# Performance work log

Measured on AMD Instinct MI355X. Metric: run time of the kernel, lower is better.

The kernel has to match this reference:

```python
import jax, jax.numpy as jnp
import numpy as np

B, T, V, E, H1, H2 = 256, 512, 50000, 300, 50, 10


def _lstm(xs, mask, W_ih, W_hh, b, hidden):
    """Masked LSTM over time-major xs [T,B,D]. mask [T,B,1]: True = valid step.
    Matches PyTorch gate order (i,f,g,o). Padded steps freeze (h,c), which is
    equivalent to pack_padded_sequence semantics (final hidden = state at last
    valid timestep)."""
    Bn = xs.shape[1]
    h0 = jnp.zeros((Bn, hidden), xs.dtype)
    c0 = jnp.zeros((Bn, hidden), xs.dtype)

    def step(carry, inp):
        h, c = carry
        x_t, m_t = inp
        g = x_t @ W_ih.T + h @ W_hh.T + b  # [B, 4H]
        i, f, gg, o = jnp.split(g, 4, axis=-1)
        c_new = jax.nn.sigmoid(f) * c + jax.nn.sigmoid(i) * jnp.tanh(gg)
        h_new = jax.nn.sigmoid(o) * jnp.tanh(c_new)
        h = jnp.where(m_t, h_new, h)
        c = jnp.where(m_t, c_new, c)
        return (h, c), h

    (hT, _), hs = jax.lax.scan(step, (h0, c0), (xs, mask))
    return hs, hT


def setup_inputs() -> dict:
    key = jax.random.key(0)
    ks = jax.random.split(key, 12)
    x = jax.random.randint(ks[0], (B, T), 0, V, dtype=jnp.int64)
    lengths = jax.random.randint(ks[1], (B,), 1, T + 1, dtype=jnp.int64)
    emb = jax.random.normal(ks[2], (V, E), dtype=jnp.float32)
    s1 = 1.0 / np.sqrt(H1)
    s2 = 1.0 / np.sqrt(H2)
    return {
        "x": x,
        "lengths": lengths,
        "emb": emb,
        "W_ih1": jax.random.uniform(ks[3], (4 * H1, E), jnp.float32, -s1, s1),
        "W_hh1": jax.random.uniform(ks[4], (4 * H1, H1), jnp.float32, -s1, s1),
        "b1": jax.random.uniform(ks[5], (4 * H1,), jnp.float32, -s1, s1),
        "W_ih2": jax.random.uniform(ks[6], (4 * H2, H1), jnp.float32, -s2, s2),
        "W_hh2": jax.random.uniform(ks[7], (4 * H2, H2), jnp.float32, -s2, s2),
        "b2": jax.random.uniform(ks[8], (4 * H2,), jnp.float32, -s2, s2),
        "fc1_w": jax.random.uniform(ks[9], (10, H2), jnp.float32, -s2, s2),
        "fc1_b": jnp.zeros((10,), jnp.float32),
        "fc2_w": jax.random.uniform(ks[10], (1, 10), jnp.float32, -s2, s2),
        "fc2_b": jnp.zeros((1,), jnp.float32),
    }


def reference(x, lengths, emb, W_ih1, W_hh1, b1, W_ih2, W_hh2, b2,
              fc1_w, fc1_b, fc2_w, fc2_b):
    e = emb[x]                                   # [B,T,E]
    xs = jnp.transpose(e, (1, 0, 2))             # time-major [T,B,E]
    mask = (jnp.arange(T)[:, None] < lengths[None, :])[..., None]  # [T,B,1]
    hs1, _ = _lstm(xs, mask, W_ih1, W_hh1, b1, H1)   # [T,B,50]
    _, h2 = _lstm(hs1, mask, W_ih2, W_hh2, b2, H2)   # final hidden [B,10]
    # dropout layers are identity in eval mode
    z = jax.nn.relu(h2 @ fc1_w.T + fc1_b)
    return z @ fc2_w.T + fc2_b                   # [B,1]
```

## Files before the change

kernel.cpp:

```cpp
#include <hip/hip_runtime.h>
#include <hip/hip_bf16.h>

#define BB 256
#define TT 512
#define EE 300
#define G4 200
#define NPAD 208
#define KP 1216
#define KC 64
#define KPD (KP/2)
#define KCD (KC/2)
#define NCH 19
#define NT 13
#define BOFF 8192
#define BUFB 34816

typedef __attribute__((ext_vector_type(8))) short short8v;
typedef __attribute__((ext_vector_type(4))) float float4v;
typedef __attribute__((ext_vector_type(4))) unsigned int uint4v;


__device__ __forceinline__ float sigm(float x) {
    return __builtin_amdgcn_rcpf(1.f + __builtin_amdgcn_exp2f(-1.442695040888963f * x));
}
__device__ __forceinline__ float tanh_(float x) {
    float t = __builtin_amdgcn_exp2f(2.885390081777927f * x);
    return 1.f - 2.f * __builtin_amdgcn_rcpf(t + 1.f);
}
template <int C>
__device__ __forceinline__ float qb(float v) {
    return __int_as_float(__builtin_amdgcn_mov_dpp(__float_as_int(v), C, 0xF, 0xF, true));
}

__device__ __forceinline__ uint2 bfsplit(float a) {
    unsigned u = __float_as_uint(a);
    unsigned rh = (u + 0x7FFFu + ((u >> 16) & 1u)) & 0xFFFF0000u;
    float l = a - __uint_as_float(rh);
    unsigned v = __float_as_uint(l);
    unsigned rl = (v + 0x7FFFu + ((v >> 16) & 1u)) >> 16;
    return make_uint2(rh >> 16, rl);
}

__global__ void wtrans_kernel(const float* __restrict__ W, const float* __restrict__ b1,
                              unsigned* __restrict__ Btg, float* __restrict__ b1p) {
    int e = blockIdx.x;
    int j = threadIdx.x;
    if (j >= NPAD) return;
    float w = 0.f;
    if (j < G4) w = W[((j & 3) * 50 + (j >> 2)) * EE + e];
    uint2 s = bfsplit(w);
    unsigned dw0 = s.x | (s.x << 16);
    unsigned dw1 = s.y | (s.y << 16);
    *(uint2*)(Btg + (size_t)j * KPD + 2 * e) = make_uint2(dw0, dw1);
    if (e == 0) b1p[j] = (j < G4) ? b1[(j & 3) * 50 + (j >> 2)] : 0.f;
}

__global__ __launch_bounds__(256, 2) void proj_kernel(
    const int* __restrict__ x, const int* __restrict__ lengths,
    const float* __restrict__ emb, const unsigned* __restrict__ Btg,
    const float* __restrict__ b1p, float* __restrict__ G1, int b0)
{
    const int b  = b0 + blockIdx.y;
    const int t0 = blockIdx.x * 64;
    const int len = lengths[b];
    if (t0 >= len) return;

    const int tid  = threadIdx.x;
    const int wv   = tid >> 6;
    const int lane = tid & 63;

    __shared__ __align__(16) char lds[2 * BUFB];

    const int arow = tid >> 2;
    const int ag   = tid & 3;
    const float* er = emb + (size_t)x[b * TT + t0 + arow] * EE;

    float4v acc[NT] = {};

    auto stageB = [&](int c, int q) {
        char* base = lds + q * BUFB + BOFF;
        #pragma unroll
        for (int rr = 0; rr < 7; ++rr) {
            if (rr < 6 || tid < 128) {
                int g   = rr * 256 + tid;
                int row = g >> 3, sl = g & 7;
                const unsigned* src = Btg + (size_t)row * KPD + c * KCD
                                      + ((sl ^ (row & 7)) << 2);
                char* dst = base + (rr * 256 + (tid & ~63)) * 16;
                __builtin_amdgcn_global_load_lds(
                    (const __attribute__((address_space(1))) void*)src,
                    (__attribute__((address_space(3))) void*)dst, 16, 0, 0);
            }
        }
    };
    auto loadA = [&](int cc) -> float4 {
        int k0 = cc * 16 + ag * 4;
        if (k0 < EE) return *(const float4*)(er + k0);
        return make_float4(0.f, 0.f, 0.f, 0.f);
    };
    auto writeA = [&](int q, float4 av) {
        uint2 s0 = bfsplit(av.x), s1 = bfsplit(av.y);
        uint2 s2 = bfsplit(av.z), s3 = bfsplit(av.w);
        unsigned p0 = s0.x | (s0.y << 16), p1 = s1.x | (s1.y << 16);
        unsigned p2 = s2.x | (s2.y << 16), p3 = s3.x | (s3.y << 16);
        char* base = lds + q * BUFB + (arow << 7);
        int r7 = arow & 7;
        *(uint4v*)(base + ((( 2 * ag    ) ^ r7) << 4)) = uint4v{p0, p0, p1, p1};
        *(uint4v*)(base + (((2 * ag + 1) ^ r7) << 4)) = uint4v{p2, p2, p3, p3};
    };

    stageB(0, 0);
    float4 aval = loadA(0);
    asm volatile("s_waitcnt vmcnt(0)" ::: "memory");
    writeA(0, aval);
    asm volatile("s_waitcnt lgkmcnt(0)" ::: "memory");
    __builtin_amdgcn_s_barrier();
    __builtin_amdgcn_sched_barrier(0);

    int p = 0;
    for (int c = 0; c < NCH; ++c) {
        const int q = p ^ 1;
        if (c + 1 < NCH) {
            stageB(c + 1, q);
            aval = loadA(c + 1);
        }
        const int r  = lane & 15;
        const int h  = lane >> 4;
        #pragma unroll
        for (int s = 0; s < 2; ++s) {
            const int sw4 = (((4 * s + h) ^ (r & 7)) << 4);
            short8v aF = *(const short8v*)(lds + p * BUFB + ((wv * 16 + r) << 7) + sw4);
            #pragma unroll
            for (int nt = 0; nt < NT; ++nt) {
                short8v bF = *(const short8v*)(lds + p * BUFB + BOFF
                                               + ((nt * 16 + r) << 7) + sw4);
                acc[nt] = __builtin_amdgcn_mfma_f32_16x16x32_bf16(aF, bF, acc[nt], 0, 0, 0);
            }
        }
        if (c + 1 < NCH) {
            asm volatile("s_waitcnt vmcnt(0)" ::: "memory");
            writeA(q, aval);
            asm volatile("s_waitcnt lgkmcnt(0)" ::: "memory");
            __builtin_amdgcn_s_barrier();
            __builtin_amdgcn_sched_barrier(0);
        }
        p = q;
    }

    float* gbase = G1 + ((size_t)blockIdx.y * TT + t0) * G4;
    const int col = lane & 15, rq = lane >> 4;
    #pragma unroll
    for (int nt = 0; nt < NT; ++nt) {
        int jp = nt * 16 + col;
        if (jp < G4) {
            float bias = b1p[jp];
            #pragma unroll
            for (int rr = 0; rr < 4; ++rr)
                gbase[(size_t)(wv * 16 + rq * 4 + rr) * G4 + jp] = acc[nt][rr] + bias;
        }
    }
}

__global__ __launch_bounds__(512, 1) void lstm_kernel(
    const int* __restrict__ lengths,
    const float* __restrict__ W_hh1, const float* __restrict__ W_ih2,
    const float* __restrict__ W_hh2, const float* __restrict__ b2,
    const float* __restrict__ fc1w, const float* __restrict__ fc1b,
    const float* __restrict__ fc2w, const float* __restrict__ fc2b,
    const float* __restrict__ G1, float* __restrict__ out, int b0)
{
    const int bb  = blockIdx.x;
    const int b   = b0 + bb;
    const int tid = threadIdx.x;
    const int len = lengths[b];

    __shared__ __align__(16) float hs[2][72];
    __shared__ __align__(16) float hfin[12];
    __shared__ float zbuf[10];

    if (tid < 72) { hs[0][tid] = 0.f; hs[1][tid] = 0.f; }

    const bool isL1 = (tid < 400);
    const bool isL2 = (tid >= 400 && tid < 480);
    const int  grp  = tid >> 3;
    const int  sub  = tid & 7;
    const int  g    = sub & 3;
    const int  half = sub >> 2;

    float wreg[28];
    float wregb[12];
    #pragma unroll
    for (int k = 0; k < 28; ++k) wreg[k] = 0.f;
    #pragma unroll
    for (int k = 0; k < 12; ++k) wregb[k] = 0.f;
    float base2 = 0.f;

    if (isL1) {
        int row = g * 50 + grp;
        const float* wp = W_hh1 + row * 50 + half * 28;
        int n = half ? 22 : 28;
        for (int k = 0; k < 28; ++k) wreg[k] = (k < n) ? wp[k] : 0.f;
    } else if (isL2) {
        int u = grp - 50;
        int row = g * 10 + u;
        const float* wp = W_ih2 + row * 50 + half * 28;
        int n = half ? 22 : 28;
        for (int k = 0; k < 28; ++k) wreg[k] = (k < n) ? wp[k] : 0.f;
        if (half == 0) {
            const float* wp2 = W_hh2 + row * 10;
            #pragma unroll
            for (int k = 0; k < 10; ++k) wregb[k] = wp2[k];
            base2 = b2[row];
        }
    }

    const bool gld  = isL1 && (half == 0);
    const int  gcol = gld ? (4 * grp + g) : 0;
    const bool wr   = (sub == 0) && (tid < 480);
    const int  slot = isL1 ? grp : (56 + grp - 50);

    float h1v[28], h2v[12];
    #pragma unroll
    for (int k = 0; k < 28; ++k) h1v[k] = 0.f;
    #pragma unroll
    for (int k = 0; k < 12; ++k) h2v[k] = 0.f;

    float c = 0.f;
    const float* g1p = G1 + (size_t)bb * TT * G4;
    float p0 = 0.f, p1 = 0.f, p2 = 0.f;
    if (gld) {
        int t1 = (1 < len) ? 1 : len - 1;
        int t2 = (2 < len) ? 2 : len - 1;
        p0 = g1p[gcol];
        p1 = g1p[(size_t)t1 * G4 + gcol];
        p2 = g1p[(size_t)t2 * G4 + gcol];
    }

    __syncthreads();

    for (int i = 0; i < len; ++i) {
        float base = gld ? p0 : ((isL2 && half == 0) ? base2 : 0.f);
        p0 = p1; p1 = p2;
        if (gld) {
            int tn = (i + 3 < len) ? i + 3 : len - 1;
            p2 = g1p[(size_t)tn * G4 + gcol];
        }

        float s0 = 0.f, s1 = 0.f, s2 = 0.f, s3 = 0.f;
        #pragma unroll
        for (int m = 0; m < 7; ++m) {
            s0 = fmaf(wreg[4*m+0], h1v[4*m+0], s0);
            s1 = fmaf(wreg[4*m+1], h1v[4*m+1], s1);
            s2 = fmaf(wreg[4*m+2], h1v[4*m+2], s2);
            s3 = fmaf(wreg[4*m+3], h1v[4*m+3], s3);
        }
        #pragma unroll
        for (int m = 0; m < 3; ++m) {
            s0 = fmaf(wregb[4*m+0], h2v[4*m+0], s0);
            s1 = fmaf(wregb[4*m+1], h2v[4*m+1], s1);
            s2 = fmaf(wregb[4*m+2], h2v[4*m+2], s2);
            s3 = fmaf(wregb[4*m+3], h2v[4*m+3], s3);
        }
        float t = base + (s0 + s1) + (s2 + s3);
        float full = t + __shfl_xor(t, 4, 64);

        float gi = qb<0x00>(full);
        float gf = qb<0x55>(full);
        float gg = qb<0xAA>(full);
        float go = qb<0xFF>(full);
        float cn = sigm(gf) * c + sigm(gi) * tanh_(gg);
        float hn = sigm(go) * tanh_(cn);
        if (isL2 && i == 0) { cn = 0.f; hn = 0.f; }
        c = cn;
        if (wr) hs[i & 1][slot] = hn;

        asm volatile("s_waitcnt lgkmcnt(0)" ::: "memory");
        __builtin_amdgcn_s_barrier();
        __builtin_amdgcn_sched_barrier(0);

        const float* hb = hs[i & 1] + half * 28;
        #pragma unroll
        for (int m = 0; m < 7; ++m) {
            float4 v = *(const float4*)(hb + 4 * m);
            h1v[4*m+0] = v.x; h1v[4*m+1] = v.y;
            h1v[4*m+2] = v.z; h1v[4*m+3] = v.w;
        }
        if (tid >= 384) {
            const float* hb2 = hs[i & 1] + 56;
            #pragma unroll
            for (int m = 0; m < 3; ++m) {
                float4 v = *(const float4*)(hb2 + 4 * m);
                h2v[4*m+0] = v.x; h2v[4*m+1] = v.y;
                h2v[4*m+2] = v.z; h2v[4*m+3] = v.w;
            }
        }
    }

    {
        float s0 = 0.f, s1 = 0.f, s2 = 0.f, s3 = 0.f;
        #pragma unroll
        for (int m = 0; m < 7; ++m) {
            s0 = fmaf(wreg[4*m+0], h1v[4*m+0], s0);
            s1 = fmaf(wreg[4*m+1], h1v[4*m+1], s1);
            s2 = fmaf(wreg[4*m+2], h1v[4*m+2], s2);
            s3 = fmaf(wreg[4*m+3], h1v[4*m+3], s3);
        }
        #pragma unroll
        for (int m = 0; m < 3; ++m) {
            s0 = fmaf(wregb[4*m+0], h2v[4*m+0], s0);
            s1 = fmaf(wregb[4*m+1], h2v[4*m+1], s1);
            s2 = fmaf(wregb[4*m+2], h2v[4*m+2], s2);
            s3 = fmaf(wregb[4*m+3], h2v[4*m+3], s3);
        }
        float t = ((isL2 && half == 0) ? base2 : 0.f) + (s0 + s1) + (s2 + s3);
        float full = t + __shfl_xor(t, 4, 64);
        float gi = qb<0x00>(full);
        float gf = qb<0x55>(full);
        float gg = qb<0xAA>(full);
        float go = qb<0xFF>(full);
        float cn = sigm(gf) * c + sigm(gi) * tanh_(gg);
        float hn = sigm(go) * tanh_(cn);
        if (isL2 && sub == 0) hfin[grp - 50] = hn;
    }
    __syncthreads();

    if (tid < 10) {
        float s = fc1b[tid];
        #pragma unroll
        for (int e = 0; e < 10; ++e) s = fmaf(fc1w[tid * 10 + e], hfin[e], s);
        zbuf[tid] = s > 0.f ? s : 0.f;
    }
    __syncthreads();
    if (tid == 0) {
        float s = fc2b[0];
        #pragma unroll
        for (int e = 0; e < 10; ++e) s = fmaf(fc2w[e], zbuf[e], s);
        out[b] = s;
    }
}

extern "C" void kernel_launch(void* const* d_in, const int* in_sizes, int n_in,
                              void* d_out, int out_size, void* d_ws, size_t ws_size,
                              hipStream_t stream)
{
    const int*   x     = (const int*)  d_in[0];
    const int*   len   = (const int*)  d_in[1];
    const float* emb   = (const float*)d_in[2];
    const float* W_ih1 = (const float*)d_in[3];
    const float* W_hh1 = (const float*)d_in[4];
    const float* b1    = (const float*)d_in[5];
    const float* W_ih2 = (const float*)d_in[6];
    const float* W_hh2 = (const float*)d_in[7];
    const float* b2    = (const float*)d_in[8];
    const float* fc1w  = (const float*)d_in[9];
    const float* fc1b  = (const float*)d_in[10];
    const float* fc2w  = (const float*)d_in[11];
    const float* fc2b  = (const float*)d_in[12];
    float* out = (float*)d_out;

    const size_t btg_bytes = (size_t)NPAD * KPD * sizeof(unsigned);
    const size_t b1p_off   = btg_bytes;
    const size_t head      = (b1p_off + NPAD * sizeof(float) + 255) & ~255ull;
    const size_t per_b     = (size_t)TT * G4 * sizeof(float);

    unsigned* Btg = (unsigned*)d_ws;
    float*    b1p = (float*)((char*)d_ws + b1p_off);
    float*    G1  = (float*)((char*)d_ws + head);

    size_t avail = ws_size > head ? ws_size - head : 0;
    int chunk = (int)(avail / per_b);
    if (chunk < 1) chunk = 1;
    if (chunk > BB) chunk = BB;

    wtrans_kernel<<<dim3(EE), dim3(256), 0, stream>>>(W_ih1, b1, Btg, b1p);

    for (int b0 = 0; b0 < BB; b0 += chunk) {
        int nb = (BB - b0) < chunk ? (BB - b0) : chunk;
        proj_kernel<<<dim3(TT / 64, nb), dim3(256), 0, stream>>>(
            x, len, emb, Btg, b1p, G1, b0);
        lstm_kernel<<<dim3(nb), dim3(512), 0, stream>>>(
            len, W_hh1, W_ih2, W_hh2, b2, fc1w, fc1b, fc2w, fc2b, G1, out, b0);
    }
}
```

Before: 318.1 us.

## Pack two sequences per LSTM block with two gate rows per thread

Restructures the recurrent LSTM kernel so that each 256-thread block processes two batch elements, one per 128-thread half. Each thread now holds two full weight rows (120 registers) and reads the hidden state directly from shared memory inside the dot product, which removes the split-K shuffle reduction and the per-step register copy of h. Gates are exchanged between thread pairs with a single quad permute. This halves the block count and lowers threads per sequence, at the cost of higher register pressure and steps run to the longer of the two lengths with masking.

```diff
diff --git a/kernel.cpp b/kernel.cpp
--- a/kernel.cpp
+++ b/kernel.cpp
@@ -161,181 +161,163 @@
     }
 }
 
-__global__ __launch_bounds__(512, 1) void lstm_kernel(
+__global__ __launch_bounds__(256, 1) void lstm_kernel(
     const int* __restrict__ lengths,
     const float* __restrict__ W_hh1, const float* __restrict__ W_ih2,
     const float* __restrict__ W_hh2, const float* __restrict__ b2,
     const float* __restrict__ fc1w, const float* __restrict__ fc1b,
     const float* __restrict__ fc2w, const float* __restrict__ fc2b,
-    const float* __restrict__ G1, float* __restrict__ out, int b0)
+    const float* __restrict__ G1, float* __restrict__ out, int b0, int nb)
 {
-    const int bb  = blockIdx.x;
-    const int b   = b0 + bb;
     const int tid = threadIdx.x;
-    const int len = lengths[b];
-
-    __shared__ __align__(16) float hs[2][72];
-    __shared__ __align__(16) float hfin[12];
-    __shared__ float zbuf[10];
-
-    if (tid < 72) { hs[0][tid] = 0.f; hs[1][tid] = 0.f; }
-
-    const bool isL1 = (tid < 400);
-    const bool isL2 = (tid >= 400 && tid < 480);
-    const int  grp  = tid >> 3;
-    const int  sub  = tid & 7;
-    const int  g    = sub & 3;
-    const int  half = sub >> 2;
-
-    float wreg[28];
-    float wregb[12];
+    const int e   = tid >> 7;
+    const int et  = tid & 127;
+    const int u   = et >> 1;
+    const int p   = et & 1;
+    const bool act  = et < 120;
+    const bool isL1 = act && (u < 50);
+    const bool isL2 = act && (u >= 50);
+
+    const int last = b0 + nb - 1;
+    int eg = b0 + blockIdx.x * 2 + e;
+    if (eg > last) eg = last;
+    const int len = lengths[eg];
+    const int ego = b0 + blockIdx.x * 2;
+    const int eg1 = (ego + 1 > last) ? last : ego + 1;
+    const int lenmax = max(lengths[ego], lengths[eg1]);
+
+    __shared__ __align__(16) float hsb[2][2][64];
+    __shared__ float hfin[2][12];
+    __shared__ float zs[2][12];
+    ((float*)hsb)[tid] = 0.f;
+
+    float wA[60], wB[60];
     #pragma unroll
-    for (int k = 0; k < 28; ++k) wreg[k] = 0.f;
-    #pragma unroll
-    for (int k = 0; k < 12; ++k) wregb[k] = 0.f;
-    float base2 = 0.f;
+    for (int k = 0; k < 60; ++k) { wA[k] = 0.f; wB[k] = 0.f; }
+    float baseA0 = 0.f, baseB0 = 0.f;
 
     if (isL1) {
-        int row = g * 50 + grp;
-        const float* wp = W_hh1 + row * 50 + half * 28;
-        int n = half ? 22 : 28;
-        for (int k = 0; k < 28; ++k) wreg[k] = (k < n) ? wp[k] : 0.f;
+        const float* a  = W_hh1 + ((2 * p) * 50 + u) * 50;
+        const float* bp = W_hh1 + ((2 * p + 1) * 50 + u) * 50;
+        #pragma unroll
+        for (int k = 0; k < 50; ++k) { wA[k] = a[k]; wB[k] = bp[k]; }
     } else if (isL2) {
-        int u = grp - 50;
-        int row = g * 10 + u;
-        const float* wp = W_ih2 + row * 50 + half * 28;
-        int n = half ? 22 : 28;
-        for (int k = 0; k < 28; ++k) wreg[k] = (k < n) ? wp[k] : 0.f;
-        if (half == 0) {
-            const float* wp2 = W_hh2 + row * 10;
-            #pragma unroll
-            for (int k = 0; k < 10; ++k) wregb[k] = wp2[k];
-            base2 = b2[row];
-        }
-    }
-
-    const bool gld  = isL1 && (half == 0);
-    const int  gcol = gld ? (4 * grp + g) : 0;
-    const bool wr   = (sub == 0) && (tid < 480);
-    const int  slot = isL1 ? grp : (56 + grp - 50);
-
-    float h1v[28], h2v[12];
-    #pragma unroll
-    for (int k = 0; k < 28; ++k) h1v[k] = 0.f;
-    #pragma unroll
-    for (int k = 0; k < 12; ++k) h2v[k] = 0.f;
-
-    float c = 0.f;
-    const float* g1p = G1 + (size_t)bb * TT * G4;
-    float p0 = 0.f, p1 = 0.f, p2 = 0.f;
-    if (gld) {
+        int u2 = u - 50;
+        int rA = (2 * p) * 10 + u2, rB = (2 * p + 1) * 10 + u2;
+        #pragma unroll
+        for (int k = 0; k < 50; ++k) { wA[k] = W_ih2[rA * 50 + k]; wB[k] = W_ih2[rB * 50 + k]; }
+        #pragma unroll
+        for (int k = 0; k < 10; ++k) { wA[50 + k] = W_hh2[rA * 10 + k]; wB[50 + k] = W_hh2[rB * 10 + k]; }
+        baseA0 = b2[rA]; baseB0 = b2[rB];
+    }
+
+    const int mylen = isL2 ? len + 1 : len;
+    const int gcol  = isL1 ? (4 * u + 2 * p) : 0;
+    const float* g1p = G1 + (size_t)(eg - b0) * TT * G4;
+
+    float2 pf0, pf1, pf2;
+    {
         int t1 = (1 < len) ? 1 : len - 1;
         int t2 = (2 < len) ? 2 : len - 1;
-        p0 = g1p[gcol];
-        p1 = g1p[(size_t)t1 * G4 + gcol];
-        p2 = g1p[(size_t)t2 * G4 + gcol];
-    }
-
+        pf0 = *(const float2*)(g1p + gcol);
+        pf1 = *(const float2*)(g1p + (size_t)t1 * G4 + gcol);
+        pf2 = *(const float2*)(g1p + (size_t)t2 * G4 + gcol);
+    }
+
+    float c = 0.f, hown = 0.f;
     __syncthreads();
 
-    for (int i = 0; i < len; ++i) {
-        float base = gld ? p0 : ((isL2 && half == 0) ? base2 : 0.f);
-        p0 = p1; p1 = p2;
-        if (gld) {
+    int pb = 0;
+    for (int i = 0; i < lenmax; ++i) {
+        float baseA = isL1 ? pf0.x : baseA0;
+        float baseB = isL1 ? pf0.y : baseB0;
+        pf0 = pf1; pf1 = pf2;
+        {
             int tn = (i + 3 < len) ? i + 3 : len - 1;
-            p2 = g1p[(size_t)tn * G4 + gcol];
-        }
-
-        float s0 = 0.f, s1 = 0.f, s2 = 0.f, s3 = 0.f;
-        #pragma unroll
-        for (int m = 0; m < 7; ++m) {
-            s0 = fmaf(wreg[4*m+0], h1v[4*m+0], s0);
-            s1 = fmaf(wreg[4*m+1], h1v[4*m+1], s1);
-            s2 = fmaf(wreg[4*m+2], h1v[4*m+2], s2);
-            s3 = fmaf(wreg[4*m+3], h1v[4*m+3], s3);
-        }
-        #pragma unroll
-        for (int m = 0; m < 3; ++m) {
-            s0 = fmaf(wregb[4*m+0], h2v[4*m+0], s0);
-            s1 = fmaf(wregb[4*m+1], h2v[4*m+1], s1);
-            s2 = fmaf(wregb[4*m+2], h2v[4*m+2], s2);
-            s3 = fmaf(wregb[4*m+3], h2v[4*m+3], s3);
-        }
-        float t = base + (s0 + s1) + (s2 + s3);
-        float full = t + __shfl_xor(t, 4, 64);
-
-        float gi = qb<0x00>(full);
-        float gf = qb<0x55>(full);
-        float gg = qb<0xAA>(full);
-        float go = qb<0xFF>(full);
+            pf2 = *(const float2*)(g1p + (size_t)tn * G4 + gcol);
+        }
+
+        float sA0 = 0.f, sA1 = 0.f, sA2 = 0.f, sA3 = 0.f;
+        float sB0 = 0.f, sB1 = 0.f, sB2 = 0.f, sB3 = 0.f;
+        const float* hb = &hsb[e][pb][0];
+        #pragma unroll
+        for (int m = 0; m < 15; ++m) {
+            float4 hv = *(const float4*)(hb + 4 * m);
+            sA0 = fmaf(wA[4*m+0], hv.x, sA0);
+            sA1 = fmaf(wA[4*m+1], hv.y, sA1);
+            sA2 = fmaf(wA[4*m+2], hv.z, sA2);
+            sA3 = fmaf(wA[4*m+3], hv.w, sA3);
+            sB0 = fmaf(wB[4*m+0], hv.x, sB0);
+            sB1 = fmaf(wB[4*m+1], hv.y, sB1);
+            sB2 = fmaf(wB[4*m+2], hv.z, sB2);
+            sB3 = fmaf(wB[4*m+3], hv.w, sB3);
+        }
+        float tA = baseA + (sA0 + sA1) + (sA2 + sA3);
+        float tB = baseB + (sB0 + sB1) + (sB2 + sB3);
+        float qA = qb<0xB1>(tA);
+        float qB = qb<0xB1>(tB);
+        float gi = p ? qA : tA;
+        float gf = p ? qB : tB;
+        float gg = p ? tA : qA;
+        float go = p ? tB : qB;
         float cn = sigm(gf) * c + sigm(gi) * tanh_(gg);
         float hn = sigm(go) * tanh_(cn);
         if (isL2 && i == 0) { cn = 0.f; hn = 0.f; }
-        c = cn;
-        if (wr) hs[i & 1][slot] = hn;
+        bool upd = (i < mylen);
+        if (upd) c = cn;
+        float hw = upd ? hn : hown;
+        hown = hw;
+        if (act && p == 0) hsb[e][pb ^ 1][u] = hw;
 
         asm volatile("s_waitcnt lgkmcnt(0)" ::: "memory");
         __builtin_amdgcn_s_barrier();
         __builtin_amdgcn_sched_barrier(0);
-
-        const float* hb = hs[i & 1] + half * 28;
-        #pragma unroll
-        for (int m = 0; m < 7; ++m) {
-            float4 v = *(const float4*)(hb + 4 * m);
-            h1v[4*m+0] = v.x; h1v[4*m+1] = v.y;
-            h1v[4*m+2] = v.z; h1v[4*m+3] = v.w;
-        }
-        if (tid >= 384) {
-            const float* hb2 = hs[i & 1] + 56;
-            #pragma unroll
-            for (int m = 0; m < 3; ++m) {
-                float4 v = *(const float4*)(hb2 + 4 * m);
-                h2v[4*m+0] = v.x; h2v[4*m+1] = v.y;
-                h2v[4*m+2] = v.z; h2v[4*m+3] = v.w;
-            }
-        }
+        pb ^= 1;
     }
 
     {
-        float s0 = 0.f, s1 = 0.f, s2 = 0.f, s3 = 0.f;
-        #pragma unroll
-        for (int m = 0; m < 7; ++m) {
-            s0 = fmaf(wreg[4*m+0], h1v[4*m+0], s0);
-            s1 = fmaf(wreg[4*m+1], h1v[4*m+1], s1);
-            s2 = fmaf(wreg[4*m+2], h1v[4*m+2], s2);
-            s3 = fmaf(wreg[4*m+3], h1v[4*m+3], s3);
-        }
-        #pragma unroll
-        for (int m = 0; m < 3; ++m) {
-            s0 = fmaf(wregb[4*m+0], h2v[4*m+0], s0);
-            s1 = fmaf(wregb[4*m+1], h2v[4*m+1], s1);
-            s2 = fmaf(wregb[4*m+2], h2v[4*m+2], s2);
-            s3 = fmaf(wregb[4*m+3], h2v[4*m+3], s3);
-        }
-        float t = ((isL2 && half == 0) ? base2 : 0.f) + (s0 + s1) + (s2 + s3);
-        float full = t + __shfl_xor(t, 4, 64);
-        float gi = qb<0x00>(full);
-        float gf = qb<0x55>(full);
-        float gg = qb<0xAA>(full);
-        float go = qb<0xFF>(full);
+        float sA0 = 0.f, sA1 = 0.f, sA2 = 0.f, sA3 = 0.f;
+        float sB0 = 0.f, sB1 = 0.f, sB2 = 0.f, sB3 = 0.f;
+        const float* hb = &hsb[e][pb][0];
+        #pragma unroll
+        for (int m = 0; m < 15; ++m) {
+            float4 hv = *(const float4*)(hb + 4 * m);
+            sA0 = fmaf(wA[4*m+0], hv.x, sA0);
+            sA1 = fmaf(wA[4*m+1], hv.y, sA1);
+            sA2 = fmaf(wA[4*m+2], hv.z, sA2);
+            sA3 = fmaf(wA[4*m+3], hv.w, sA3);
+            sB0 = fmaf(wB[4*m+0], hv.x, sB0);
+            sB1 = fmaf(wB[4*m+1], hv.y, sB1);
+            sB2 = fmaf(wB[4*m+2], hv.z, sB2);
+            sB3 = fmaf(wB[4*m+3], hv.w, sB3);
+        }
+        float tA = baseA0 + (sA0 + sA1) + (sA2 + sA3);
+        float tB = baseB0 + (sB0 + sB1) + (sB2 + sB3);
+        float qA = qb<0xB1>(tA);
+        float qB = qb<0xB1>(tB);
+        float gi = p ? qA : tA;
+        float gf = p ? qB : tB;
+        float gg = p ? tA : qA;
+        float go = p ? tB : qB;
         float cn = sigm(gf) * c + sigm(gi) * tanh_(gg);
         float hn = sigm(go) * tanh_(cn);
-        if (isL2 && sub == 0) hfin[grp - 50] = hn;
+        float h2f = (len == lenmax) ? hn : hown;
+        if (isL2 && p == 0) hfin[e][u - 50] = h2f;
     }
     __syncthreads();
 
-    if (tid < 10) {
-        float s = fc1b[tid];
-        #pragma unroll
-        for (int e = 0; e < 10; ++e) s = fmaf(fc1w[tid * 10 + e], hfin[e], s);
-        zbuf[tid] = s > 0.f ? s : 0.f;
+    if (et < 10) {
+        float s = fc1b[et];
+        #pragma unroll
+        for (int k = 0; k < 10; ++k) s = fmaf(fc1w[et * 10 + k], hfin[e][k], s);
+        zs[e][et] = s > 0.f ? s : 0.f;
     }
     __syncthreads();
-    if (tid == 0) {
+    if (et == 0) {
         float s = fc2b[0];
         #pragma unroll
-        for (int e = 0; e < 10; ++e) s = fmaf(fc2w[e], zbuf[e], s);
-        out[b] = s;
+        for (int k = 0; k < 10; ++k) s = fmaf(fc2w[k], zs[e][k], s);
+        out[eg] = s;
     }
 }
 
@@ -378,7 +360,7 @@
         int nb = (BB - b0) < chunk ? (BB - b0) : chunk;
         proj_kernel<<<dim3(TT / 64, nb), dim3(256), 0, stream>>>(
             x, len, emb, Btg, b1p, G1, b0);
-        lstm_kernel<<<dim3(nb), dim3(512), 0, stream>>>(
-            len, W_hh1, W_ih2, W_hh2, b2, fc1w, fc1b, fc2w, fc2b, G1, out, b0);
-    }
-}
+        lstm_kernel<<<dim3((nb + 1) / 2), dim3(256), 0, stream>>>(
+            len, W_hh1, W_ih2, W_hh2, b2, fc1w, fc1b, fc2w, fc2b, G1, out, b0, nb);
+    }
+}
```

New measurement: 440.8 us. 38.5% more time.

## Give each LSTM gate row to one thread and halve the recurrence block size

Applied to the files above, without the earlier changes.

The recurrent kernel now runs 256 threads per sequence instead of 512. Each thread holds a full 50-wide weight row in registers, so the cross-lane shuffle that combined two half-row partial sums disappears. The per-step barrier now spans four waves instead of eight, which should shorten the serial latency of each timestep. In exchange each thread does twice as many FMAs per step and uses more registers for weights and hidden-state copies.

```diff
diff --git a/kernel.cpp b/kernel.cpp
--- a/kernel.cpp
+++ b/kernel.cpp
@@ -49,9 +49,8 @@
     float w = 0.f;
     if (j < G4) w = W[((j & 3) * 50 + (j >> 2)) * EE + e];
     uint2 s = bfsplit(w);
-    unsigned dw0 = s.x | (s.x << 16);
-    unsigned dw1 = s.y | (s.y << 16);
-    *(uint2*)(Btg + (size_t)j * KPD + 2 * e) = make_uint2(dw0, dw1);
+    *(uint2*)(Btg + (size_t)j * KPD + 2 * e) =
+        make_uint2(s.x | (s.x << 16), s.y | (s.y << 16));
     if (e == 0) b1p[j] = (j < G4) ? b1[(j & 3) * 50 + (j >> 2)] : 0.f;
 }
 
@@ -161,7 +160,7 @@
     }
 }
 
-__global__ __launch_bounds__(512, 1) void lstm_kernel(
+__global__ __launch_bounds__(256, 1) void lstm_kernel(
     const int* __restrict__ lengths,
     const float* __restrict__ W_hh1, const float* __restrict__ W_ih2,
     const float* __restrict__ W_hh2, const float* __restrict__ b2,
@@ -174,81 +173,72 @@
     const int tid = threadIdx.x;
     const int len = lengths[b];
 
-    __shared__ __align__(16) float hs[2][72];
+    __shared__ __align__(16) float hs[2][64];
     __shared__ __align__(16) float hfin[12];
     __shared__ float zbuf[10];
 
-    if (tid < 72) { hs[0][tid] = 0.f; hs[1][tid] = 0.f; }
-
-    const bool isL1 = (tid < 400);
-    const bool isL2 = (tid >= 400 && tid < 480);
-    const int  grp  = tid >> 3;
-    const int  sub  = tid & 7;
-    const int  g    = sub & 3;
-    const int  half = sub >> 2;
-
-    float wreg[28];
+    if (tid < 64) { hs[0][tid] = 0.f; hs[1][tid] = 0.f; }
+
+    const bool isL1 = (tid < 200);
+    const bool isL2 = (tid >= 200 && tid < 240);
+
+    float wreg[52];
     float wregb[12];
     #pragma unroll
-    for (int k = 0; k < 28; ++k) wreg[k] = 0.f;
+    for (int k = 0; k < 52; ++k) wreg[k] = 0.f;
     #pragma unroll
     for (int k = 0; k < 12; ++k) wregb[k] = 0.f;
     float base2 = 0.f;
 
     if (isL1) {
-        int row = g * 50 + grp;
-        const float* wp = W_hh1 + row * 50 + half * 28;
-        int n = half ? 22 : 28;
-        for (int k = 0; k < 28; ++k) wreg[k] = (k < n) ? wp[k] : 0.f;
+        int u = tid >> 2, g = tid & 3;
+        const float* wp = W_hh1 + (g * 50 + u) * 50;
+        #pragma unroll
+        for (int k = 0; k < 50; ++k) wreg[k] = wp[k];
     } else if (isL2) {
-        int u = grp - 50;
+        int q = tid - 200, u = q >> 2, g = q & 3;
         int row = g * 10 + u;
-        const float* wp = W_ih2 + row * 50 + half * 28;
-        int n = half ? 22 : 28;
-        for (int k = 0; k < 28; ++k) wreg[k] = (k < n) ? wp[k] : 0.f;
-        if (half == 0) {
-            const float* wp2 = W_hh2 + row * 10;
-            #pragma unroll
-            for (int k = 0; k < 10; ++k) wregb[k] = wp2[k];
-            base2 = b2[row];
-        }
-    }
-
-    const bool gld  = isL1 && (half == 0);
-    const int  gcol = gld ? (4 * grp + g) : 0;
-    const bool wr   = (sub == 0) && (tid < 480);
-    const int  slot = isL1 ? grp : (56 + grp - 50);
-
-    float h1v[28], h2v[12];
-    #pragma unroll
-    for (int k = 0; k < 28; ++k) h1v[k] = 0.f;
+        const float* wp = W_ih2 + row * 50;
+        #pragma unroll
+        for (int k = 0; k < 50; ++k) wreg[k] = wp[k];
+        const float* wp2 = W_hh2 + row * 10;
+        #pragma unroll
+        for (int k = 0; k < 10; ++k) wregb[k] = wp2[k];
+        base2 = b2[row];
+    }
+
+    const bool wr   = ((tid & 3) == 0) && (tid < 240);
+    const int  slot = isL1 ? (tid >> 2) : (52 + ((tid - 200) >> 2));
+
+    float h1v[52], h2v[12];
+    #pragma unroll
+    for (int k = 0; k < 52; ++k) h1v[k] = 0.f;
     #pragma unroll
     for (int k = 0; k < 12; ++k) h2v[k] = 0.f;
 
     float c = 0.f;
     const float* g1p = G1 + (size_t)bb * TT * G4;
-    float p0 = 0.f, p1 = 0.f, p2 = 0.f;
-    if (gld) {
+    const int gcol = isL1 ? tid : 199;
+    float g0, g1r, g2r;
+    {
         int t1 = (1 < len) ? 1 : len - 1;
         int t2 = (2 < len) ? 2 : len - 1;
-        p0 = g1p[gcol];
-        p1 = g1p[(size_t)t1 * G4 + gcol];
-        p2 = g1p[(size_t)t2 * G4 + gcol];
+        g0  = g1p[gcol];
+        g1r = g1p[(size_t)t1 * G4 + gcol];
+        g2r = g1p[(size_t)t2 * G4 + gcol];
     }
 
     __syncthreads();
 
     for (int i = 0; i < len; ++i) {
-        float base = gld ? p0 : ((isL2 && half == 0) ? base2 : 0.f);
-        p0 = p1; p1 = p2;
-        if (gld) {
-            int tn = (i + 3 < len) ? i + 3 : len - 1;
-            p2 = g1p[(size_t)tn * G4 + gcol];
-        }
+        float base = isL1 ? g0 : base2;
+        g0 = g1r; g1r = g2r;
+        int tn = (i + 3 < len) ? i + 3 : len - 1;
+        g2r = g1p[(size_t)tn * G4 + gcol];
 
         float s0 = 0.f, s1 = 0.f, s2 = 0.f, s3 = 0.f;
         #pragma unroll
-        for (int m = 0; m < 7; ++m) {
+        for (int m = 0; m < 13; ++m) {
             s0 = fmaf(wreg[4*m+0], h1v[4*m+0], s0);
             s1 = fmaf(wreg[4*m+1], h1v[4*m+1], s1);
             s2 = fmaf(wreg[4*m+2], h1v[4*m+2], s2);
@@ -261,13 +251,12 @@
             s2 = fmaf(wregb[4*m+2], h2v[4*m+2], s2);
             s3 = fmaf(wregb[4*m+3], h2v[4*m+3], s3);
         }
-        float t = base + (s0 + s1) + (s2 + s3);
-        float full = t + __shfl_xor(t, 4, 64);
-
-        float gi = qb<0x00>(full);
-        float gf = qb<0x55>(full);
-        float gg = qb<0xAA>(full);
-        float go = qb<0xFF>(full);
+        float gv = base + (s0 + s1) + (s2 + s3);
+
+        float gi = qb<0x00>(gv);
+        float gf = qb<0x55>(gv);
+        float gg = qb<0xAA>(gv);
+        float go = qb<0xFF>(gv);
         float cn = sigm(gf) * c + sigm(gi) * tanh_(gg);
         float hn = sigm(go) * tanh_(cn);
         if (isL2 && i == 0) { cn = 0.f; hn = 0.f; }
@@ -278,28 +267,27 @@
         __builtin_amdgcn_s_barrier();
         __builtin_amdgcn_sched_barrier(0);
 
-        const float* hb = hs[i & 1] + half * 28;
-        #pragma unroll
-        for (int m = 0; m < 7; ++m) {
+        const float* hb = hs[i & 1];
+        #pragma unroll
+        for (int m = 0; m < 13; ++m) {
             float4 v = *(const float4*)(hb + 4 * m);
             h1v[4*m+0] = v.x; h1v[4*m+1] = v.y;
             h1v[4*m+2] = v.z; h1v[4*m+3] = v.w;
         }
-        if (tid >= 384) {
-            const float* hb2 = hs[i & 1] + 56;
+        if (tid >= 192) {
             #pragma unroll
             for (int m = 0; m < 3; ++m) {
-                float4 v = *(const float4*)(hb2 + 4 * m);
+                float4 v = *(const float4*)(hb + 52 + 4 * m);
                 h2v[4*m+0] = v.x; h2v[4*m+1] = v.y;
                 h2v[4*m+2] = v.z; h2v[4*m+3] = v.w;
             }
         }
     }
 
-    {
+    if (isL2) {
         float s0 = 0.f, s1 = 0.f, s2 = 0.f, s3 = 0.f;
         #pragma unroll
-        for (int m = 0; m < 7; ++m) {
+        for (int m = 0; m < 13; ++m) {
             s0 = fmaf(wreg[4*m+0], h1v[4*m+0], s0);
             s1 = fmaf(wreg[4*m+1], h1v[4*m+1], s1);
             s2 = fmaf(wreg[4*m+2], h1v[4*m+2], s2);
@@ -312,15 +300,14 @@
             s2 = fmaf(wregb[4*m+2], h2v[4*m+2], s2);
             s3 = fmaf(wregb[4*m+3], h2v[4*m+3], s3);
         }
-        float t = ((isL2 && half == 0) ? base2 : 0.f) + (s0 + s1) + (s2 + s3);
-        float full = t + __shfl_xor(t, 4, 64);
-        float gi = qb<0x00>(full);
-        float gf = qb<0x55>(full);
-        float gg = qb<0xAA>(full);
-        float go = qb<0xFF>(full);
+        float gv = base2 + (s0 + s1) + (s2 + s3);
+        float gi = qb<0x00>(gv);
+        float gf = qb<0x55>(gv);
+        float gg = qb<0xAA>(gv);
+        float go = qb<0xFF>(gv);
         float cn = sigm(gf) * c + sigm(gi) * tanh_(gg);
         float hn = sigm(go) * tanh_(cn);
-        if (isL2 && sub == 0) hfin[grp - 50] = hn;
+        if ((tid & 3) == 0) hfin[(tid - 200) >> 2] = hn;
     }
     __syncthreads();
 
@@ -359,9 +346,9 @@
     float* out = (float*)d_out;
 
     const size_t btg_bytes = (size_t)NPAD * KPD * sizeof(unsigned);
-    const size_t b1p_off   = btg_bytes;
-    const size_t head      = (b1p_off + NPAD * sizeof(float) + 255) & ~255ull;
-    const size_t per_b     = (size_t)TT * G4 * sizeof(float);
+    const size_t b1p_off = btg_bytes;
+    const size_t head = (b1p_off + NPAD * sizeof(float) + 255) & ~255ull;
+    const size_t per_b = (size_t)TT * G4 * sizeof(float);
 
     unsigned* Btg = (unsigned*)d_ws;
     float*    b1p = (float*)((char*)d_ws + b1p_off);
@@ -378,7 +365,7 @@
         int nb = (BB - b0) < chunk ? (BB - b0) : chunk;
         proj_kernel<<<dim3(TT / 64, nb), dim3(256), 0, stream>>>(
             x, len, emb, Btg, b1p, G1, b0);
-        lstm_kernel<<<dim3(nb), dim3(512), 0, stream>>>(
+        lstm_kernel<<<dim3(nb), dim3(256), 0, stream>>>(
             len, W_hh1, W_ih2, W_hh2, b2, fc1w, fc1b, fc2w, fc2b, G1, out, b0);
     }
 }
```

Result: slower. 347.7 us (+9.3%).
